# Kernel optimization log

Measured on AMD Instinct MI355X. Metric: run time of the kernel, lower is better.

Reference implementation:

```python
import jax, jax.numpy as jnp
import numpy as np


def setup_inputs() -> dict:
    key = jax.random.key(0)
    k1, k2, k3 = jax.random.split(key, 3)
    N1, N2, P, D = 4, 8, 1024, 128  # P = PH*PW = 32*32 (512px / 16 patch)
    feats = jax.random.normal(k1, (N1, P, D), dtype=jnp.float32)
    nfeats = jax.random.normal(k2, (N2, P, D), dtype=jnp.float32)
    background_masks = jax.random.uniform(k3, (N1, P), dtype=jnp.float32)
    return {"feats": feats, "nfeats": nfeats, "background_masks": background_masks,
            "PH": 32, "PW": 32, "H": 512, "W": 512}


def reference(feats, nfeats, background_masks, PH, PW, H, W):
    # L2-normalize patch embeddings (as in `f / f.norm(dim=-1, keepdim=True)`)
    f = feats / jnp.linalg.norm(feats, axis=-1, keepdims=True)    # [N1,P,D]
    g = nfeats / jnp.linalg.norm(nfeats, axis=-1, keepdims=True)  # [N2,Q,D]
    # Euclidean cdist of unit vectors: d^2 = 2 - 2*dot (clamped at 0)
    dot = jnp.einsum('npd,mqd->nmpq', f, g)                        # [N1,N2,P,Q]
    dist = jnp.sqrt(jnp.maximum(2.0 - 2.0 * dot, 0.0)) / 2.0      # cdist/2, permuted
    # min over normal patches Q -> per-query-patch nearest-neighbor distance
    scores_patch = dist.min(axis=-1)                               # [N1,N2,P]
    scores_patch = scores_patch * background_masks[:, None, :]
    # image score: max over query patches, mean over normal images
    scores = scores_patch.max(axis=-1).mean(axis=-1)               # [N1]
    # pixel map: mean over normal images, reshape to patch grid, bilinear upsample
    sp = scores_patch.mean(axis=1).reshape(-1, PH, PW)             # [N1,PH,PW]
    scores_pixel = jax.image.resize(sp, (sp.shape[0], H, W), method='bilinear')
    return scores, scores_pixel
```

## Files before the change

kernel.cpp:

```cpp
#include <hip/hip_runtime.h>

typedef __attribute__((ext_vector_type(8))) short short8;
typedef __attribute__((ext_vector_type(4))) float f32x4;

typedef const __attribute__((address_space(1))) unsigned int glb_u32;
typedef __attribute__((address_space(3))) unsigned int lds_u32;

static __device__ inline unsigned short f2bf(float x) {
    unsigned int u = __float_as_uint(x);
    u = (u + 0x7FFFu + ((u >> 16) & 1u)) >> 16;
    return (unsigned short)u;
}

__global__ __launch_bounds__(256) void knorm(const float* __restrict__ feats,
                                             const float* __restrict__ nfeats,
                                             unsigned short* __restrict__ fb,
                                             unsigned short* __restrict__ gb) {
    int row = blockIdx.x * 4 + (threadIdx.x >> 6);
    int lane = threadIdx.x & 63;
    const float* src;
    unsigned short* dst;
    if (row < 4096) { src = feats + row * 128;           dst = fb + row * 128; }
    else            { src = nfeats + (row - 4096) * 128; dst = gb + (row - 4096) * 128; }
    float2 v = ((const float2*)src)[lane];
    float ss = v.x * v.x + v.y * v.y;
    #pragma unroll
    for (int d = 32; d; d >>= 1) ss += __shfl_xor(ss, d);
    float inv = 1.0f / sqrtf(ss);
    ushort2 o;
    o.x = f2bf(v.x * inv);
    o.y = f2bf(v.y * inv);
    ((ushort2*)dst)[lane] = o;
}

__global__ __launch_bounds__(512, 4) void kscore(const unsigned short* __restrict__ fb,
                                                 const unsigned short* __restrict__ gb,
                                                 float* __restrict__ sp_part) {
    __shared__ unsigned short gtile[6][32 * 128];
    const int tid = threadIdx.x;
    const int lane = tid & 63;
    const int wave = tid >> 6;
    const int wp = wave >> 1, wqt = wave & 1;
    const int l15 = lane & 15, lhi = lane >> 4;
    const int m = blockIdx.x;
    const int ptile = blockIdx.y >> 2, qq = blockIdx.y & 3;
    const int rowbase = ptile * 256 + wp * 64;

    const unsigned short* gBase = gb + ((size_t)m * 1024 + qq * 256) * 128;

    short8 a[4][4];
    #pragma unroll
    for (int pg = 0; pg < 4; pg++) {
        const unsigned short* arow = fb + (size_t)(rowbase + pg * 16 + l15) * 128;
        #pragma unroll
        for (int kk = 0; kk < 4; kk++)
            a[pg][kk] = *(const short8*)(arow + kk * 32 + lhi * 8);
    }
    __builtin_amdgcn_sched_barrier(0);

    auto stage = [&](int buf, int qb) {
        int r = tid >> 4, s = tid & 15;
        int scol = s ^ (r & 7);
        __builtin_amdgcn_global_load_lds(
            (glb_u32*)(gBase + (size_t)(qb + r) * 128 + scol * 8),
            (lds_u32*)((char*)gtile[buf] + tid * 16), 16, 0, 0);
    };

    stage(0, 0); stage(1, 32); stage(2, 64); stage(3, 96); stage(4, 128);

    f32x4 mx[4];
    #pragma unroll
    for (int pg = 0; pg < 4; pg++)
        #pragma unroll
        for (int i = 0; i < 4; i++) mx[pg][i] = -1e30f;

    #pragma unroll
    for (int t = 0; t < 8; t++) {
        if (t < 4)       asm volatile("s_waitcnt vmcnt(4)" ::: "memory");
        else if (t == 4) asm volatile("s_waitcnt vmcnt(3)" ::: "memory");
        else if (t == 5) asm volatile("s_waitcnt vmcnt(2)" ::: "memory");
        else if (t == 6) asm volatile("s_waitcnt vmcnt(1)" ::: "memory");
        else             asm volatile("s_waitcnt vmcnt(0)" ::: "memory");
        __builtin_amdgcn_s_barrier();
        __builtin_amdgcn_sched_barrier(0);
        if (t < 3) stage((t + 5) % 6, (t + 5) * 32);
        const char* tp = (const char*)gtile[t % 6];
        const int r = wqt * 16 + l15;
        const int rowoff = r * 256;
        const int swz = (r & 7) << 4;
        f32x4 acc[4];
        #pragma unroll
        for (int pg = 0; pg < 4; pg++)
            #pragma unroll
            for (int i = 0; i < 4; i++) acc[pg][i] = 0.f;
        #pragma unroll
        for (int kk = 0; kk < 4; kk++) {
            short8 b = *(const short8*)(tp + ((rowoff + kk * 64 + lhi * 16) ^ swz));
            #pragma unroll
            for (int pg = 0; pg < 4; pg++)
                acc[pg] = __builtin_amdgcn_mfma_f32_16x16x32_bf16(a[pg][kk], b, acc[pg], 0, 0, 0);
        }
        #pragma unroll
        for (int pg = 0; pg < 4; pg++)
            #pragma unroll
            for (int i = 0; i < 4; i++) mx[pg][i] = fmaxf(mx[pg][i], acc[pg][i]);
    }

    #pragma unroll
    for (int pg = 0; pg < 4; pg++)
        #pragma unroll
        for (int i = 0; i < 4; i++) {
            float v = mx[pg][i];
            v = fmaxf(v, __shfl_xor(v, 1));
            v = fmaxf(v, __shfl_xor(v, 2));
            v = fmaxf(v, __shfl_xor(v, 4));
            v = fmaxf(v, __shfl_xor(v, 8));
            mx[pg][i] = v;
        }
    if (l15 == 0) {
        const int slot = qq * 2 + wqt;
        #pragma unroll
        for (int pg = 0; pg < 4; pg++)
            #pragma unroll
            for (int i = 0; i < 4; i++) {
                int row = rowbase + pg * 16 + lhi * 4 + i;
                int n = row >> 10, p = row & 1023;
                sp_part[((size_t)(n * 8 + m) * 8 + slot) * 1024 + p] = mx[pg][i];
            }
    }
}

__global__ __launch_bounds__(256) void kfinal(const float* __restrict__ sp_part,
                                              const float* __restrict__ mask,
                                              float* __restrict__ out) {
    const int n = blockIdx.y;
    const int bx = blockIdx.x;
    const int t = threadIdx.x;
    float* pix = out + 4;

    if (bx == 64) {
        __shared__ float smax[4];
        float acc = 0.f;
        for (int m = 0; m < 8; m++) {
            const float* base = sp_part + (size_t)(n * 8 + m) * 8 * 1024;
            float lm = -1e30f;
            #pragma unroll
            for (int i = 0; i < 4; i++) {
                int p = i * 256 + t;
                float dot = -1e30f;
                #pragma unroll
                for (int s = 0; s < 8; s++) dot = fmaxf(dot, base[s * 1024 + p]);
                float d = sqrtf(fmaxf(2.0f - 2.0f * dot, 0.0f)) * 0.5f * mask[n * 1024 + p];
                lm = fmaxf(lm, d);
            }
            #pragma unroll
            for (int d = 32; d; d >>= 1) lm = fmaxf(lm, __shfl_xor(lm, d));
            if ((t & 63) == 0) smax[t >> 6] = lm;
            __syncthreads();
            if (t == 0) acc += fmaxf(fmaxf(smax[0], smax[1]), fmaxf(smax[2], smax[3]));
            __syncthreads();
        }
        if (t == 0) out[n] = acc * 0.125f;
        return;
    }

    __shared__ float sp_row[2][32];
    const int band = bx * 8;
    const int pr_lo = (int)floorf((band + 0.5f) * 0.0625f - 0.5f);
    const int row0 = min(max(pr_lo, 0), 31);
    const int row1 = min(max(pr_lo + 1, 0), 31);
    {
        int v = t >> 2, sub = t & 3;
        int vr = v >> 5, vc = v & 31;
        int p = (vr ? row1 : row0) * 32 + vc;
        float sum = 0.f;
        #pragma unroll
        for (int mi = 0; mi < 2; mi++) {
            int m = sub * 2 + mi;
            const float* base = sp_part + (size_t)(n * 8 + m) * 8 * 1024 + p;
            float dot = -1e30f;
            #pragma unroll
            for (int s = 0; s < 8; s++) dot = fmaxf(dot, base[s * 1024]);
            sum += sqrtf(fmaxf(2.0f - 2.0f * dot, 0.0f)) * 0.5f;
        }
        sum *= mask[n * 1024 + p];
        sum += __shfl_xor(sum, 1);
        sum += __shfl_xor(sum, 2);
        if (sub == 0) sp_row[vr][vc] = sum * 0.125f;
    }
    __syncthreads();
    #pragma unroll
    for (int i = 0; i < 16; i++) {
        int idx = i * 256 + t;
        int yl = idx >> 9, x = idx & 511;
        int y = band + yl;
        float fy = (y + 0.5f) * 0.0625f - 0.5f;
        float ty = fy - (float)pr_lo;
        float fx = (x + 0.5f) * 0.0625f - 0.5f;
        float xf = floorf(fx);
        float tx = fx - xf;
        int x0 = (int)xf;
        int x0c = min(max(x0, 0), 31), x1c = min(max(x0 + 1, 0), 31);
        float v00 = sp_row[0][x0c], v01 = sp_row[0][x1c];
        float v10 = sp_row[1][x0c], v11 = sp_row[1][x1c];
        float v0 = v00 + tx * (v01 - v00);
        float v1 = v10 + tx * (v11 - v10);
        pix[(size_t)n * 262144 + (size_t)y * 512 + x] = v0 + ty * (v1 - v0);
    }
}

extern "C" void kernel_launch(void* const* d_in, const int* in_sizes, int n_in,
                              void* d_out, int out_size, void* d_ws, size_t ws_size,
                              hipStream_t stream) {
    const float* feats = (const float*)d_in[0];
    const float* nfeats = (const float*)d_in[1];
    const float* mask = (const float*)d_in[2];
    float* out = (float*)d_out;

    unsigned short* fb = (unsigned short*)d_ws;
    unsigned short* gb = fb + 4096 * 128;
    float* sp_part = (float*)((char*)d_ws + 3u * 1024u * 1024u);

    knorm<<<3072, 256, 0, stream>>>(feats, nfeats, fb, gb);
    kscore<<<dim3(8, 64), 512, 0, stream>>>(fb, gb, sp_part);
    kfinal<<<dim3(65, 4), 256, 0, stream>>>(sp_part, mask, out);
}
```

Measured before the change: 36.49 us.

## Drop LDS staging in kscore; load B fragments directly from global

The score kernel no longer stages normal-feature tiles into shared memory through a six-buffer async pipeline with barriers. Instead each wave reads its own 128-row Q slice directly from global memory into registers as MFMA B operands. The grid is reshaped to 256-thread blocks over (m, n*pgroup, 2 q-halves), so each wave owns one of eight Q slices. This removes LDS traffic and block barriers, but loses the block-level sharing of B tiles, so global and L2 traffic goes up and load latency is exposed.

```diff
diff --git a/kernel.cpp b/kernel.cpp
--- a/kernel.cpp
+++ b/kernel.cpp
@@ -2,9 +2,6 @@
 
 typedef __attribute__((ext_vector_type(8))) short short8;
 typedef __attribute__((ext_vector_type(4))) float f32x4;
-
-typedef const __attribute__((address_space(1))) unsigned int glb_u32;
-typedef __attribute__((address_space(3))) unsigned int lds_u32;
 
 static __device__ inline unsigned short f2bf(float x) {
     unsigned int u = __float_as_uint(x);
@@ -33,40 +30,28 @@
     ((ushort2*)dst)[lane] = o;
 }
 
-__global__ __launch_bounds__(512, 4) void kscore(const unsigned short* __restrict__ fb,
+__global__ __launch_bounds__(256, 3) void kscore(const unsigned short* __restrict__ fb,
                                                  const unsigned short* __restrict__ gb,
                                                  float* __restrict__ sp_part) {
-    __shared__ unsigned short gtile[6][32 * 128];
     const int tid = threadIdx.x;
     const int lane = tid & 63;
-    const int wave = tid >> 6;
-    const int wp = wave >> 1, wqt = wave & 1;
+    const int w = tid >> 6;
     const int l15 = lane & 15, lhi = lane >> 4;
     const int m = blockIdx.x;
-    const int ptile = blockIdx.y >> 2, qq = blockIdx.y & 3;
-    const int rowbase = ptile * 256 + wp * 64;
-
-    const unsigned short* gBase = gb + ((size_t)m * 1024 + qq * 256) * 128;
+    const int n = blockIdx.y >> 4, pgb = blockIdx.y & 15;
+    const int qs = blockIdx.z * 4 + w;
+    const int p0 = pgb * 64;
 
     short8 a[4][4];
     #pragma unroll
     for (int pg = 0; pg < 4; pg++) {
-        const unsigned short* arow = fb + (size_t)(rowbase + pg * 16 + l15) * 128;
+        const unsigned short* arow = fb + (size_t)(n * 1024 + p0 + pg * 16 + l15) * 128;
         #pragma unroll
         for (int kk = 0; kk < 4; kk++)
             a[pg][kk] = *(const short8*)(arow + kk * 32 + lhi * 8);
     }
-    __builtin_amdgcn_sched_barrier(0);
-
-    auto stage = [&](int buf, int qb) {
-        int r = tid >> 4, s = tid & 15;
-        int scol = s ^ (r & 7);
-        __builtin_amdgcn_global_load_lds(
-            (glb_u32*)(gBase + (size_t)(qb + r) * 128 + scol * 8),
-            (lds_u32*)((char*)gtile[buf] + tid * 16), 16, 0, 0);
-    };
-
-    stage(0, 0); stage(1, 32); stage(2, 64); stage(3, 96); stage(4, 128);
+
+    const unsigned short* gBase = gb + ((size_t)m * 1024 + qs * 128) * 128 + lhi * 8;
 
     f32x4 mx[4];
     #pragma unroll
@@ -75,30 +60,21 @@
         for (int i = 0; i < 4; i++) mx[pg][i] = -1e30f;
 
     #pragma unroll
-    for (int t = 0; t < 8; t++) {
-        if (t < 4)       asm volatile("s_waitcnt vmcnt(4)" ::: "memory");
-        else if (t == 4) asm volatile("s_waitcnt vmcnt(3)" ::: "memory");
-        else if (t == 5) asm volatile("s_waitcnt vmcnt(2)" ::: "memory");
-        else if (t == 6) asm volatile("s_waitcnt vmcnt(1)" ::: "memory");
-        else             asm volatile("s_waitcnt vmcnt(0)" ::: "memory");
-        __builtin_amdgcn_s_barrier();
-        __builtin_amdgcn_sched_barrier(0);
-        if (t < 3) stage((t + 5) % 6, (t + 5) * 32);
-        const char* tp = (const char*)gtile[t % 6];
-        const int r = wqt * 16 + l15;
-        const int rowoff = r * 256;
-        const int swz = (r & 7) << 4;
+    for (int qt = 0; qt < 8; qt++) {
+        const unsigned short* grow = gBase + (size_t)(qt * 16 + l15) * 128;
+        short8 b0 = *(const short8*)(grow);
+        short8 b1 = *(const short8*)(grow + 32);
+        short8 b2 = *(const short8*)(grow + 64);
+        short8 b3 = *(const short8*)(grow + 96);
         f32x4 acc[4];
         #pragma unroll
-        for (int pg = 0; pg < 4; pg++)
+        for (int pg = 0; pg < 4; pg++) {
             #pragma unroll
             for (int i = 0; i < 4; i++) acc[pg][i] = 0.f;
-        #pragma unroll
-        for (int kk = 0; kk < 4; kk++) {
-            short8 b = *(const short8*)(tp + ((rowoff + kk * 64 + lhi * 16) ^ swz));
-            #pragma unroll
-            for (int pg = 0; pg < 4; pg++)
-                acc[pg] = __builtin_amdgcn_mfma_f32_16x16x32_bf16(a[pg][kk], b, acc[pg], 0, 0, 0);
+            acc[pg] = __builtin_amdgcn_mfma_f32_16x16x32_bf16(a[pg][0], b0, acc[pg], 0, 0, 0);
+            acc[pg] = __builtin_amdgcn_mfma_f32_16x16x32_bf16(a[pg][1], b1, acc[pg], 0, 0, 0);
+            acc[pg] = __builtin_amdgcn_mfma_f32_16x16x32_bf16(a[pg][2], b2, acc[pg], 0, 0, 0);
+            acc[pg] = __builtin_amdgcn_mfma_f32_16x16x32_bf16(a[pg][3], b3, acc[pg], 0, 0, 0);
         }
         #pragma unroll
         for (int pg = 0; pg < 4; pg++)
@@ -118,14 +94,12 @@
             mx[pg][i] = v;
         }
     if (l15 == 0) {
-        const int slot = qq * 2 + wqt;
         #pragma unroll
         for (int pg = 0; pg < 4; pg++)
             #pragma unroll
             for (int i = 0; i < 4; i++) {
-                int row = rowbase + pg * 16 + lhi * 4 + i;
-                int n = row >> 10, p = row & 1023;
-                sp_part[((size_t)(n * 8 + m) * 8 + slot) * 1024 + p] = mx[pg][i];
+                int p = p0 + pg * 16 + lhi * 4 + i;
+                sp_part[((size_t)(n * 8 + m) * 8 + qs) * 1024 + p] = mx[pg][i];
             }
     }
 }
@@ -222,6 +196,6 @@
     float* sp_part = (float*)((char*)d_ws + 3u * 1024u * 1024u);
 
     knorm<<<3072, 256, 0, stream>>>(feats, nfeats, fb, gb);
-    kscore<<<dim3(8, 64), 512, 0, stream>>>(fb, gb, sp_part);
+    kscore<<<dim3(8, 64, 2), 256, 0, stream>>>(fb, gb, sp_part);
     kfinal<<<dim3(65, 4), 256, 0, stream>>>(sp_part, mask, out);
 }
```

After: 43.53 us. 1.19x slower.

## Shrink LDS ring to triple buffer and restructure kscore pipeline with setprio

Applied to the files above, without the earlier changes.

The kscore staging ring goes from six 8 KB LDS buffers to three, with a two-tile prefetch distance. The wait and barrier now sit at the end of each iteration instead of the start. All four B fragments are loaded up front and the MFMA chain runs under raised wave priority, with the accumulation order changed to run over pg then kk. Cutting LDS from 48 KB to 24 KB per block can raise occupancy, but the shallower prefetch leaves less global latency hidden.

```diff
diff --git a/kernel.cpp b/kernel.cpp
--- a/kernel.cpp
+++ b/kernel.cpp
@@ -36,7 +36,7 @@
 __global__ __launch_bounds__(512, 4) void kscore(const unsigned short* __restrict__ fb,
                                                  const unsigned short* __restrict__ gb,
                                                  float* __restrict__ sp_part) {
-    __shared__ unsigned short gtile[6][32 * 128];
+    __shared__ char gtile[3][8192];
     const int tid = threadIdx.x;
     const int lane = tid & 63;
     const int wave = tid >> 6;
@@ -63,10 +63,11 @@
         int scol = s ^ (r & 7);
         __builtin_amdgcn_global_load_lds(
             (glb_u32*)(gBase + (size_t)(qb + r) * 128 + scol * 8),
-            (lds_u32*)((char*)gtile[buf] + tid * 16), 16, 0, 0);
+            (lds_u32*)(gtile[buf] + tid * 16), 16, 0, 0);
     };
 
-    stage(0, 0); stage(1, 32); stage(2, 64); stage(3, 96); stage(4, 128);
+    stage(0, 0);
+    stage(1, 32);
 
     f32x4 mx[4];
     #pragma unroll
@@ -74,36 +75,42 @@
         #pragma unroll
         for (int i = 0; i < 4; i++) mx[pg][i] = -1e30f;
 
+    asm volatile("s_waitcnt vmcnt(1)" ::: "memory");
+    __builtin_amdgcn_s_barrier();
+
     #pragma unroll
     for (int t = 0; t < 8; t++) {
-        if (t < 4)       asm volatile("s_waitcnt vmcnt(4)" ::: "memory");
-        else if (t == 4) asm volatile("s_waitcnt vmcnt(3)" ::: "memory");
-        else if (t == 5) asm volatile("s_waitcnt vmcnt(2)" ::: "memory");
-        else if (t == 6) asm volatile("s_waitcnt vmcnt(1)" ::: "memory");
-        else             asm volatile("s_waitcnt vmcnt(0)" ::: "memory");
-        __builtin_amdgcn_s_barrier();
+        if (t + 2 < 8) stage((t + 2) % 3, (t + 2) * 32);
         __builtin_amdgcn_sched_barrier(0);
-        if (t < 3) stage((t + 5) % 6, (t + 5) * 32);
-        const char* tp = (const char*)gtile[t % 6];
+        const char* tp = gtile[t % 3];
         const int r = wqt * 16 + l15;
         const int rowoff = r * 256;
         const int swz = (r & 7) << 4;
+        short8 b0 = *(const short8*)(tp + ((rowoff +   0 + lhi * 16) ^ swz));
+        short8 b1 = *(const short8*)(tp + ((rowoff +  64 + lhi * 16) ^ swz));
+        short8 b2 = *(const short8*)(tp + ((rowoff + 128 + lhi * 16) ^ swz));
+        short8 b3 = *(const short8*)(tp + ((rowoff + 192 + lhi * 16) ^ swz));
+        asm volatile("s_waitcnt lgkmcnt(0)" ::: "memory");
+        __builtin_amdgcn_sched_barrier(0);
+        __builtin_amdgcn_s_setprio(1);
         f32x4 acc[4];
         #pragma unroll
+        for (int pg = 0; pg < 4; pg++) {
+            #pragma unroll
+            for (int i = 0; i < 4; i++) acc[pg][i] = 0.f;
+            acc[pg] = __builtin_amdgcn_mfma_f32_16x16x32_bf16(a[pg][0], b0, acc[pg], 0, 0, 0);
+            acc[pg] = __builtin_amdgcn_mfma_f32_16x16x32_bf16(a[pg][1], b1, acc[pg], 0, 0, 0);
+            acc[pg] = __builtin_amdgcn_mfma_f32_16x16x32_bf16(a[pg][2], b2, acc[pg], 0, 0, 0);
+            acc[pg] = __builtin_amdgcn_mfma_f32_16x16x32_bf16(a[pg][3], b3, acc[pg], 0, 0, 0);
+        }
+        __builtin_amdgcn_s_setprio(0);
+        #pragma unroll
         for (int pg = 0; pg < 4; pg++)
             #pragma unroll
-            for (int i = 0; i < 4; i++) acc[pg][i] = 0.f;
-        #pragma unroll
-        for (int kk = 0; kk < 4; kk++) {
-            short8 b = *(const short8*)(tp + ((rowoff + kk * 64 + lhi * 16) ^ swz));
-            #pragma unroll
-            for (int pg = 0; pg < 4; pg++)
-                acc[pg] = __builtin_amdgcn_mfma_f32_16x16x32_bf16(a[pg][kk], b, acc[pg], 0, 0, 0);
-        }
-        #pragma unroll
-        for (int pg = 0; pg < 4; pg++)
-            #pragma unroll
             for (int i = 0; i < 4; i++) mx[pg][i] = fmaxf(mx[pg][i], acc[pg][i]);
+        if (t < 6)      asm volatile("s_waitcnt vmcnt(1)" ::: "memory");
+        else if (t == 6) asm volatile("s_waitcnt vmcnt(0)" ::: "memory");
+        if (t < 7) __builtin_amdgcn_s_barrier();
     }
 
     #pragma unroll
```

New measurement: 37.99 us. +4.1%, slower.
